# Kernel tuning notes

Measured on AMD Instinct MI355X. Metric: run time of the kernel, lower is better.

## Reference

```python
import jax, jax.numpy as jnp
import numpy as np

N, E, EL, D_IN, D_H = 100000, 1600000, 200000, 128, 128

def setup_inputs() -> dict:
    key = jax.random.key(0)
    ks = jax.random.split(key, 12)
    glorot = lambda k, fi, fo: jax.random.normal(k, (fi, fo), jnp.float32) * np.sqrt(2.0 / (fi + fo))
    return {
        "x": jax.random.normal(ks[0], (N, D_IN), jnp.float32),
        "edge_index": jax.random.randint(ks[1], (2, E), 0, N, jnp.int64),
        "edge_label_index": jax.random.randint(ks[2], (2, EL), 0, N, jnp.int64),
        "W1": glorot(ks[3], D_IN, D_H), "b1": jnp.zeros((D_H,), jnp.float32),
        "W2": glorot(ks[4], D_H, D_H), "b2": jnp.zeros((D_H,), jnp.float32),
        "Wp1": glorot(ks[5], 2 * D_H, D_H), "bp1": jnp.zeros((D_H,), jnp.float32),
        "Wp2": glorot(ks[6], D_H, 1), "bp2": jnp.zeros((1,), jnp.float32),
    }

def gcn_conv(x, W, b, src, dst, n_nodes):
    # GCNConv: h = D^{-1/2} (A + I) D^{-1/2} (x @ W) + b, deg includes self-loop
    h = x @ W                                            # [N, D]
    deg = jnp.zeros((n_nodes,), h.dtype).at[dst].add(1.0) + 1.0
    dinv = jax.lax.rsqrt(deg)                            # [N]
    coef = dinv[src] * dinv[dst]                         # [E]
    agg = jnp.zeros_like(h).at[dst].add(h[src] * coef[:, None])
    agg = agg + h * (dinv * dinv)[:, None]               # self-loop term
    return agg + b

def reference(x, edge_index, edge_label_index, W1, b1, W2, b2, Wp1, bp1, Wp2, bp2):
    src, dst = edge_index[0], edge_index[1]
    n = x.shape[0]
    h = jax.nn.relu(gcn_conv(x, W1, b1, src, dst, n))
    h = gcn_conv(h, W2, b2, src, dst, n)
    # link scoring: gather src/dst embeddings, concat, 2-layer MLP (dropout = eval identity)
    edge_emb = jnp.concatenate([h[edge_label_index[0]], h[edge_label_index[1]]], axis=1)  # [EL, 2D]
    pred = jax.nn.relu(edge_emb @ Wp1 + bp1) @ Wp2 + bp2
    return pred.squeeze(-1)
```

## Files before the change

kernel.cpp:

```cpp
#include <hip/hip_runtime.h>

#define NN 100000
#define EE 1600000
#define ELN 200000

#define NB 98
#define BKT_SHIFT 10
#define BKT_NODES 1024
#define MSB 256
#define EPB (EE / MSB)

typedef __attribute__((ext_vector_type(4))) float f32x4;
typedef __attribute__((ext_vector_type(8))) short short8;

__device__ __forceinline__ unsigned short f2bf(float f) {
    unsigned u = __builtin_bit_cast(unsigned, f);
    u += 0x7FFF + ((u >> 16) & 1);
    return (unsigned short)(u >> 16);
}
__device__ __forceinline__ float bf2f(unsigned short h) {
    return __builtin_bit_cast(float, (unsigned)h << 16);
}

__device__ __forceinline__ void convw_one(const float* __restrict__ W,
                                          unsigned short* __restrict__ WT, int K, int u) {
    int n = u & 127, kq = u >> 7;
    short8 t;
#pragma unroll
    for (int j = 0; j < 8; j++)
        t[j] = (short)f2bf(W[(size_t)(kq * 8 + j) * 128 + n]);
    *(short8*)(WT + (size_t)n * K + kq * 8) = t;
}

__global__ __launch_bounds__(256) void convw_kernel(const float* __restrict__ W1,
                                                    const float* __restrict__ W2,
                                                    const float* __restrict__ Wp1,
                                                    unsigned short* __restrict__ W1T,
                                                    unsigned short* __restrict__ W2T,
                                                    unsigned short* __restrict__ WpT) {
    int u = blockIdx.x * 256 + threadIdx.x;
    if (u < 2048) convw_one(W1, W1T, 128, u);
    else if (u < 4096) convw_one(W2, W2T, 128, u - 2048);
    else convw_one(Wp1, WpT, 256, u - 4096);
}

__global__ __launch_bounds__(256) void ms_hist_kernel(const int* __restrict__ dst,
                                                      int* __restrict__ histM) {
    __shared__ int cnt[NB];
    int tid = threadIdx.x;
    if (tid < NB) cnt[tid] = 0;
    __syncthreads();
    int base = blockIdx.x * EPB;
    for (int i = tid; i < EPB; i += 256)
        atomicAdd(&cnt[dst[base + i] >> BKT_SHIFT], 1);
    __syncthreads();
    if (tid < NB) histM[tid * MSB + blockIdx.x] = cnt[tid];
}

__global__ __launch_bounds__(256) void ms_scan_kernel(int* __restrict__ histM,
                                                      int* __restrict__ rowptr) {
    __shared__ int sm[256];
    int tid = threadIdx.x;
    const int CPT = NB * MSB / 256;
    int base = tid * CPT;
    int s = 0;
    for (int i = 0; i < CPT; i++) s += histM[base + i];
    sm[tid] = s;
    __syncthreads();
    for (int off = 1; off < 256; off <<= 1) {
        int add = (tid >= off) ? sm[tid - off] : 0;
        __syncthreads();
        sm[tid] += add;
        __syncthreads();
    }
    int run = sm[tid] - s;
    for (int i = 0; i < CPT; i++) {
        int v = histM[base + i];
        histM[base + i] = run;
        run += v;
    }
    if (tid == 0) rowptr[NN] = EE;
}

__global__ __launch_bounds__(256) void ms_scatter_kernel(const int* __restrict__ src,
                                                         const int* __restrict__ dst,
                                                         const int* __restrict__ histO,
                                                         unsigned* __restrict__ tmp) {
    __shared__ int off[NB];
    int tid = threadIdx.x;
    if (tid < NB) off[tid] = histO[tid * MSB + blockIdx.x];
    __syncthreads();
    int base = blockIdx.x * EPB;
    for (int i = tid; i < EPB; i += 256) {
        int d = dst[base + i];
        int s = src[base + i];
        int b = d >> BKT_SHIFT;
        int pos = atomicAdd(&off[b], 1);
        tmp[pos] = ((unsigned)(d & (BKT_NODES - 1)) << 17) | (unsigned)s;
    }
}

__global__ __launch_bounds__(256) void bucket_csr_kernel(const unsigned* __restrict__ tmp,
                                                         const int* __restrict__ histO,
                                                         int* __restrict__ rowptr,
                                                         float* __restrict__ dinv,
                                                         int* __restrict__ csr) {
    __shared__ int cnt[BKT_NODES];
    __shared__ int lp[BKT_NODES];
    __shared__ int sm[256];
    int b = blockIdx.x;
    int tid = threadIdx.x;
    int gbase = histO[b * MSB];
    int gend = (b == NB - 1) ? EE : histO[(b + 1) * MSB];
    for (int i = tid; i < BKT_NODES; i += 256) cnt[i] = 0;
    __syncthreads();
    for (int i = gbase + tid; i < gend; i += 256)
        atomicAdd(&cnt[tmp[i] >> 17], 1);
    __syncthreads();
    int s0 = cnt[tid * 4], s1 = cnt[tid * 4 + 1], s2 = cnt[tid * 4 + 2], s3 = cnt[tid * 4 + 3];
    int tot = s0 + s1 + s2 + s3;
    sm[tid] = tot;
    __syncthreads();
    for (int off = 1; off < 256; off <<= 1) {
        int add = (tid >= off) ? sm[tid - off] : 0;
        __syncthreads();
        sm[tid] += add;
        __syncthreads();
    }
    int excl = sm[tid] - tot;
    lp[tid * 4] = excl;
    lp[tid * 4 + 1] = excl + s0;
    lp[tid * 4 + 2] = excl + s0 + s1;
    lp[tid * 4 + 3] = excl + s0 + s1 + s2;
    int n0 = b << BKT_SHIFT;
#pragma unroll
    for (int q = 0; q < 4; q++) {
        int i = tid * 4 + q;
        int node = n0 + i;
        if (node < NN) {
            rowptr[node] = gbase + (q == 0 ? excl : lp[i]);
            int c = (q == 0) ? s0 : (q == 1 ? s1 : (q == 2 ? s2 : s3));
            dinv[node] = rsqrtf((float)c + 1.0f);
        }
    }
    cnt[tid * 4] = 0; cnt[tid * 4 + 1] = 0; cnt[tid * 4 + 2] = 0; cnt[tid * 4 + 3] = 0;
    __syncthreads();
    for (int i = gbase + tid; i < gend; i += 256) {
        unsigned p = tmp[i];
        int dl = p >> 17;
        int s = p & 0x1FFFF;
        int pos = atomicAdd(&cnt[dl], 1);
        csr[gbase + lp[dl] + pos] = s;
    }
}

template <bool A_IS_F32>
__global__ __launch_bounds__(256) void gemm_mfma_kernel(const void* __restrict__ Av,
                                                        const unsigned short* __restrict__ WT,
                                                        unsigned short* __restrict__ out,
                                                        int nrows, int nchunks) {
    __shared__ __align__(16) char Wl[128 * 128 * 2];
    int tid = threadIdx.x;
#pragma unroll
    for (int j = 0; j < 8; j++) {
        int slot = tid + j * 256;
        int n = slot >> 4, k0 = (slot & 15) * 8;
        int byte = (n * 256 + k0 * 2) ^ ((n & 7) << 4);
        *(short8*)(Wl + byte) = ((const short8*)WT)[slot];
    }
    __syncthreads();
    int wid = tid >> 6, l = tid & 63;
    int lhi = l >> 4, llo = l & 15;
    for (int chunk = blockIdx.x; chunk < nchunks; chunk += gridDim.x) {
        int r0 = chunk * 64 + wid * 16;
        int arow = r0 + llo;
        f32x4 acc[8];
#pragma unroll
        for (int c = 0; c < 8; c++) acc[c] = (f32x4)0.0f;
#pragma unroll
        for (int ks = 0; ks < 4; ks++) {
            int koff = ks * 32 + lhi * 8;
            short8 a;
            if (arow < nrows) {
                if (A_IS_F32) {
                    const float* ap = (const float*)Av + (size_t)arow * 128 + koff;
                    float4 v0 = *(const float4*)ap;
                    float4 v1 = *(const float4*)(ap + 4);
                    a[0] = (short)f2bf(v0.x); a[1] = (short)f2bf(v0.y);
                    a[2] = (short)f2bf(v0.z); a[3] = (short)f2bf(v0.w);
                    a[4] = (short)f2bf(v1.x); a[5] = (short)f2bf(v1.y);
                    a[6] = (short)f2bf(v1.z); a[7] = (short)f2bf(v1.w);
                } else {
                    a = *(const short8*)((const unsigned short*)Av + (size_t)arow * 128 + koff);
                }
            } else {
                a = (short8)(short)0;
            }
#pragma unroll
            for (int c = 0; c < 8; c++) {
                int n = c * 16 + llo;
                int byte = (n * 256 + koff * 2) ^ ((n & 7) << 4);
                short8 bfr = *(const short8*)(Wl + byte);
                acc[c] = __builtin_amdgcn_mfma_f32_16x16x32_bf16(a, bfr, acc[c], 0, 0, 0);
            }
        }
#pragma unroll
        for (int c = 0; c < 8; c++) {
            int col = c * 16 + llo;
#pragma unroll
            for (int j = 0; j < 4; j++) {
                int row = r0 + lhi * 4 + j;
                if (row < nrows) out[(size_t)row * 128 + col] = f2bf(acc[c][j]);
            }
        }
    }
}

__global__ __launch_bounds__(256) void agg_bf16_kernel(const unsigned short* __restrict__ h,
                                                       const int* __restrict__ rowptr,
                                                       const int* __restrict__ csr,
                                                       const float* __restrict__ dinv,
                                                       const float* __restrict__ bias,
                                                       unsigned short* __restrict__ out,
                                                       int relu) {
    int wid = threadIdx.x >> 6, l = threadIdx.x & 63;
    int node = blockIdx.x * 4 + wid;
    if (node >= NN) return;
    const unsigned* hp = (const unsigned*)h;
    float dn = dinv[node];
    unsigned sv = hp[(size_t)node * 64 + l];
    float a0 = bf2f((unsigned short)sv) * dn * dn;
    float a1 = bf2f((unsigned short)(sv >> 16)) * dn * dn;
    int beg = rowptr[node], end = rowptr[node + 1];
    int i = beg;
    for (; i + 8 <= end; i += 8) {
        int s[8];
        unsigned v[8];
        float c[8];
#pragma unroll
        for (int j = 0; j < 8; j++) s[j] = __builtin_nontemporal_load(csr + i + j);
#pragma unroll
        for (int j = 0; j < 8; j++) v[j] = hp[(size_t)s[j] * 64 + l];
#pragma unroll
        for (int j = 0; j < 8; j++) c[j] = dinv[s[j]] * dn;
#pragma unroll
        for (int j = 0; j < 8; j++) {
            a0 += c[j] * bf2f((unsigned short)v[j]);
            a1 += c[j] * bf2f((unsigned short)(v[j] >> 16));
        }
    }
    for (; i < end; i++) {
        int s = __builtin_nontemporal_load(csr + i);
        unsigned v = hp[(size_t)s * 64 + l];
        float c = dinv[s] * dn;
        a0 += c * bf2f((unsigned short)v);
        a1 += c * bf2f((unsigned short)(v >> 16));
    }
    a0 += bias[l * 2];
    a1 += bias[l * 2 + 1];
    if (relu) { a0 = fmaxf(a0, 0.f); a1 = fmaxf(a1, 0.f); }
    unsigned packed = (unsigned)f2bf(a0) | ((unsigned)f2bf(a1) << 16);
    __builtin_nontemporal_store(packed, (unsigned*)out + (size_t)node * 64 + l);
}

__global__ __launch_bounds__(512, 2) void link_mfma_kernel(const unsigned short* __restrict__ h,
                                                           const int* __restrict__ eli,
                                                           const unsigned short* __restrict__ WpT,
                                                           const float* __restrict__ bp1,
                                                           const float* __restrict__ Wp2,
                                                           const float* __restrict__ bp2,
                                                           float* __restrict__ out) {
    __shared__ __align__(16) char Wl[128 * 256 * 2];
    int tid = threadIdx.x;
#pragma unroll
    for (int j = 0; j < 8; j++) {
        int slot = tid + j * 512;
        int n = slot >> 5, k0 = (slot & 31) * 8;
        int byte = (n * 512 + k0 * 2) ^ ((n & 7) << 4);
        *(short8*)(Wl + byte) = ((const short8*)WpT)[slot];
    }
    __syncthreads();
    int wid = tid >> 6, l = tid & 63;
    int lhi = l >> 4, llo = l & 15;
    float b2 = bp2[0];
    const int NG = (ELN + 127) / 128;
    for (int g = blockIdx.x; g < NG; g += gridDim.x) {
        int e_base = g * 128 + wid * 16;
        if (e_base >= ELN) continue;
        int ea = e_base + llo;
        int es = eli[ea], et = eli[ELN + ea];
        f32x4 acc[8];
#pragma unroll
        for (int c = 0; c < 8; c++) acc[c] = (f32x4)0.0f;
#pragma unroll
        for (int ks = 0; ks < 8; ks++) {
            int kg = ks * 32 + lhi * 8;
            int row = (kg < 128) ? es : et;
            int koff = kg & 127;
            short8 a = *(const short8*)(h + (size_t)row * 128 + koff);
#pragma unroll
            for (int c = 0; c < 8; c++) {
                int n = c * 16 + llo;
                int byte = (n * 512 + kg * 2) ^ ((n & 7) << 4);
                short8 bfr = *(const short8*)(Wl + byte);
                acc[c] = __builtin_amdgcn_mfma_f32_16x16x32_bf16(a, bfr, acc[c], 0, 0, 0);
            }
        }
        float p0 = 0.f, p1 = 0.f, p2 = 0.f, p3 = 0.f;
#pragma unroll
        for (int c = 0; c < 8; c++) {
            int col = c * 16 + llo;
            float bb = bp1[col];
            float w2 = Wp2[col];
            p0 += fmaxf(acc[c][0] + bb, 0.f) * w2;
            p1 += fmaxf(acc[c][1] + bb, 0.f) * w2;
            p2 += fmaxf(acc[c][2] + bb, 0.f) * w2;
            p3 += fmaxf(acc[c][3] + bb, 0.f) * w2;
        }
#pragma unroll
        for (int off = 1; off < 16; off <<= 1) {
            p0 += __shfl_xor(p0, off);
            p1 += __shfl_xor(p1, off);
            p2 += __shfl_xor(p2, off);
            p3 += __shfl_xor(p3, off);
        }
        if (llo == 0) {
            int e = e_base + lhi * 4;
            out[e + 0] = p0 + b2;
            out[e + 1] = p1 + b2;
            out[e + 2] = p2 + b2;
            out[e + 3] = p3 + b2;
        }
    }
}

extern "C" void kernel_launch(void* const* d_in, const int* in_sizes, int n_in,
                              void* d_out, int out_size, void* d_ws, size_t ws_size,
                              hipStream_t stream) {
    const float* x   = (const float*)d_in[0];
    const int*   ei  = (const int*)d_in[1];
    const int*   eli = (const int*)d_in[2];
    const float* W1  = (const float*)d_in[3];
    const float* b1  = (const float*)d_in[4];
    const float* W2  = (const float*)d_in[5];
    const float* b2  = (const float*)d_in[6];
    const float* Wp1 = (const float*)d_in[7];
    const float* bp1 = (const float*)d_in[8];
    const float* Wp2 = (const float*)d_in[9];
    const float* bp2 = (const float*)d_in[10];
    float* out = (float*)d_out;

    char* w = (char*)d_ws;
    auto alloc = [&](size_t bytes) {
        char* p = w;
        w += (bytes + 255) & ~(size_t)255;
        return p;
    };
    float*          dinv   = (float*)alloc((size_t)NN * 4);
    int*            rowptr = (int*)alloc((size_t)(NN + 1) * 4);
    int*            histM  = (int*)alloc((size_t)NB * MSB * 4);
    unsigned*       tmp    = (unsigned*)alloc((size_t)EE * 4);
    int*            csr    = (int*)alloc((size_t)EE * 4);
    unsigned short* hA     = (unsigned short*)alloc((size_t)NN * 128 * 2);
    unsigned short* hB     = (unsigned short*)alloc((size_t)NN * 128 * 2);
    unsigned short* W1T    = (unsigned short*)alloc((size_t)128 * 128 * 2);
    unsigned short* W2T    = (unsigned short*)alloc((size_t)128 * 128 * 2);
    unsigned short* WpT    = (unsigned short*)alloc((size_t)128 * 256 * 2);

    const int* srcv = ei;
    const int* dstv = ei + EE;

    convw_kernel<<<32, 256, 0, stream>>>(W1, W2, Wp1, W1T, W2T, WpT);

    ms_hist_kernel<<<MSB, 256, 0, stream>>>(dstv, histM);
    ms_scan_kernel<<<1, 256, 0, stream>>>(histM, rowptr);
    ms_scatter_kernel<<<MSB, 256, 0, stream>>>(srcv, dstv, histM, tmp);
    bucket_csr_kernel<<<NB, 256, 0, stream>>>(tmp, histM, rowptr, dinv, csr);

    int nchunks = (NN + 63) / 64;
    gemm_mfma_kernel<true><<<1024, 256, 0, stream>>>(x, W1T, hA, NN, nchunks);
    agg_bf16_kernel<<<NN / 4, 256, 0, stream>>>(hA, rowptr, csr, dinv, b1, hB, 1);
    gemm_mfma_kernel<false><<<1024, 256, 0, stream>>>(hB, W2T, hA, NN, nchunks);
    agg_bf16_kernel<<<NN / 4, 256, 0, stream>>>(hA, rowptr, csr, dinv, b2, hB, 0);
    link_mfma_kernel<<<512, 512, 0, stream>>>(hB, eli, WpT, bp1, Wp2, bp2, out);
}
```

Baseline: 330.3 us.

## Pre-scale GEMM output by dinv and aggregate over feature-sliced layout

```diff
diff --git a/kernel.cpp b/kernel.cpp
--- a/kernel.cpp
+++ b/kernel.cpp
@@ -154,11 +154,12 @@
     }
 }
 
-template <bool A_IS_F32>
+template <int AMODE>
 __global__ __launch_bounds__(256) void gemm_mfma_kernel(const void* __restrict__ Av,
                                                         const unsigned short* __restrict__ WT,
+                                                        const float* __restrict__ dinv,
                                                         unsigned short* __restrict__ out,
-                                                        int nrows, int nchunks) {
+                                                        int nchunks) {
     __shared__ __align__(16) char Wl[128 * 128 * 2];
     int tid = threadIdx.x;
 #pragma unroll
@@ -181,8 +182,8 @@
         for (int ks = 0; ks < 4; ks++) {
             int koff = ks * 32 + lhi * 8;
             short8 a;
-            if (arow < nrows) {
-                if (A_IS_F32) {
+            if (arow < NN) {
+                if (AMODE == 0) {
                     const float* ap = (const float*)Av + (size_t)arow * 128 + koff;
                     float4 v0 = *(const float4*)ap;
                     float4 v1 = *(const float4*)(ap + 4);
@@ -191,7 +192,9 @@
                     a[4] = (short)f2bf(v1.x); a[5] = (short)f2bf(v1.y);
                     a[6] = (short)f2bf(v1.z); a[7] = (short)f2bf(v1.w);
                 } else {
-                    a = *(const short8*)((const unsigned short*)Av + (size_t)arow * 128 + koff);
+                    const unsigned short* gsrc = (const unsigned short*)Av;
+                    a = *(const short8*)(gsrc + (size_t)(koff >> 4) * (NN * 16) +
+                                         (size_t)arow * 16 + (koff & 15));
                 }
             } else {
                 a = (short8)(short)0;
@@ -204,63 +207,75 @@
                 acc[c] = __builtin_amdgcn_mfma_f32_16x16x32_bf16(a, bfr, acc[c], 0, 0, 0);
             }
         }
+        float dv[4];
+#pragma unroll
+        for (int j = 0; j < 4; j++) {
+            int row = r0 + lhi * 4 + j;
+            dv[j] = (row < NN) ? dinv[row] : 0.f;
+        }
 #pragma unroll
         for (int c = 0; c < 8; c++) {
-            int col = c * 16 + llo;
 #pragma unroll
             for (int j = 0; j < 4; j++) {
                 int row = r0 + lhi * 4 + j;
-                if (row < nrows) out[(size_t)row * 128 + col] = f2bf(acc[c][j]);
+                if (row < NN)
+                    out[(size_t)c * (NN * 16) + (size_t)row * 16 + llo] = f2bf(acc[c][j] * dv[j]);
             }
         }
     }
 }
 
-__global__ __launch_bounds__(256) void agg_bf16_kernel(const unsigned short* __restrict__ h,
-                                                       const int* __restrict__ rowptr,
-                                                       const int* __restrict__ csr,
-                                                       const float* __restrict__ dinv,
-                                                       const float* __restrict__ bias,
-                                                       unsigned short* __restrict__ out,
-                                                       int relu) {
-    int wid = threadIdx.x >> 6, l = threadIdx.x & 63;
-    int node = blockIdx.x * 4 + wid;
-    if (node >= NN) return;
-    const unsigned* hp = (const unsigned*)h;
-    float dn = dinv[node];
-    unsigned sv = hp[(size_t)node * 64 + l];
-    float a0 = bf2f((unsigned short)sv) * dn * dn;
-    float a1 = bf2f((unsigned short)(sv >> 16)) * dn * dn;
-    int beg = rowptr[node], end = rowptr[node + 1];
-    int i = beg;
-    for (; i + 8 <= end; i += 8) {
-        int s[8];
-        unsigned v[8];
-        float c[8];
-#pragma unroll
-        for (int j = 0; j < 8; j++) s[j] = __builtin_nontemporal_load(csr + i + j);
-#pragma unroll
-        for (int j = 0; j < 8; j++) v[j] = hp[(size_t)s[j] * 64 + l];
-#pragma unroll
-        for (int j = 0; j < 8; j++) c[j] = dinv[s[j]] * dn;
-#pragma unroll
-        for (int j = 0; j < 8; j++) {
-            a0 += c[j] * bf2f((unsigned short)v[j]);
-            a1 += c[j] * bf2f((unsigned short)(v[j] >> 16));
-        }
-    }
-    for (; i < end; i++) {
-        int s = __builtin_nontemporal_load(csr + i);
-        unsigned v = hp[(size_t)s * 64 + l];
-        float c = dinv[s] * dn;
-        a0 += c * bf2f((unsigned short)v);
-        a1 += c * bf2f((unsigned short)(v >> 16));
-    }
-    a0 += bias[l * 2];
-    a1 += bias[l * 2 + 1];
-    if (relu) { a0 = fmaxf(a0, 0.f); a1 = fmaxf(a1, 0.f); }
-    unsigned packed = (unsigned)f2bf(a0) | ((unsigned)f2bf(a1) << 16);
-    __builtin_nontemporal_store(packed, (unsigned*)out + (size_t)node * 64 + l);
+template <int OUT_ROW>
+__global__ __launch_bounds__(512) void agg_fs_kernel(const unsigned short* __restrict__ g,
+                                                     const int* __restrict__ rowptr,
+                                                     const int* __restrict__ csr,
+                                                     const float* __restrict__ dinv,
+                                                     const float* __restrict__ bias,
+                                                     unsigned short* __restrict__ out) {
+    int s = blockIdx.x & 7;
+    int nb = blockIdx.x >> 3;
+    int w = threadIdx.x >> 6;
+    int l = threadIdx.x & 63;
+    int j = l >> 3, d = l & 7;
+    const unsigned* gp = (const unsigned*)g + (size_t)s * (NN * 8);
+    float bb0 = bias[s * 16 + d * 2];
+    float bb1 = bias[s * 16 + d * 2 + 1];
+#pragma unroll
+    for (int t = 0; t < 4; t++) {
+        int node = nb * 32 + w * 4 + t;
+        float a0 = 0.f, a1 = 0.f;
+        int beg = rowptr[node], end = rowptr[node + 1];
+        for (int i = beg + j; i < end; i += 16) {
+            int s0 = csr[i];
+            int i1 = i + 8;
+            int s1 = (i1 < end) ? csr[i1] : -1;
+            unsigned v0 = gp[(size_t)s0 * 8 + d];
+            a0 += bf2f((unsigned short)v0);
+            a1 += bf2f((unsigned short)(v0 >> 16));
+            if (s1 >= 0) {
+                unsigned v1 = gp[(size_t)s1 * 8 + d];
+                a0 += bf2f((unsigned short)v1);
+                a1 += bf2f((unsigned short)(v1 >> 16));
+            }
+        }
+        a0 += __shfl_xor(a0, 8);  a1 += __shfl_xor(a1, 8);
+        a0 += __shfl_xor(a0, 16); a1 += __shfl_xor(a1, 16);
+        a0 += __shfl_xor(a0, 32); a1 += __shfl_xor(a1, 32);
+        unsigned sv = gp[(size_t)node * 8 + d];
+        a0 += bf2f((unsigned short)sv);
+        a1 += bf2f((unsigned short)(sv >> 16));
+        float dn = dinv[node];
+        a0 = fmaf(dn, a0, bb0);
+        a1 = fmaf(dn, a1, bb1);
+        if (!OUT_ROW) { a0 = fmaxf(a0, 0.f); a1 = fmaxf(a1, 0.f); }
+        if (j == 0) {
+            unsigned packed = (unsigned)f2bf(a0) | ((unsigned)f2bf(a1) << 16);
+            if (OUT_ROW)
+                ((unsigned*)out)[(size_t)node * 64 + s * 8 + d] = packed;
+            else
+                ((unsigned*)out)[(size_t)s * (NN * 8) + (size_t)node * 8 + d] = packed;
+        }
+    }
 }
 
 __global__ __launch_bounds__(512, 2) void link_mfma_kernel(const unsigned short* __restrict__ h,
@@ -361,8 +376,8 @@
     int*            histM  = (int*)alloc((size_t)NB * MSB * 4);
     unsigned*       tmp    = (unsigned*)alloc((size_t)EE * 4);
     int*            csr    = (int*)alloc((size_t)EE * 4);
-    unsigned short* hA     = (unsigned short*)alloc((size_t)NN * 128 * 2);
-    unsigned short* hB     = (unsigned short*)alloc((size_t)NN * 128 * 2);
+    unsigned short* gbuf   = (unsigned short*)alloc((size_t)NN * 128 * 2);
+    unsigned short* hbuf   = (unsigned short*)alloc((size_t)NN * 128 * 2);
     unsigned short* W1T    = (unsigned short*)alloc((size_t)128 * 128 * 2);
     unsigned short* W2T    = (unsigned short*)alloc((size_t)128 * 128 * 2);
     unsigned short* WpT    = (unsigned short*)alloc((size_t)128 * 256 * 2);
@@ -378,9 +393,9 @@
     bucket_csr_kernel<<<NB, 256, 0, stream>>>(tmp, histM, rowptr, dinv, csr);
 
     int nchunks = (NN + 63) / 64;
-    gemm_mfma_kernel<true><<<1024, 256, 0, stream>>>(x, W1T, hA, NN, nchunks);
-    agg_bf16_kernel<<<NN / 4, 256, 0, stream>>>(hA, rowptr, csr, dinv, b1, hB, 1);
-    gemm_mfma_kernel<false><<<1024, 256, 0, stream>>>(hB, W2T, hA, NN, nchunks);
-    agg_bf16_kernel<<<NN / 4, 256, 0, stream>>>(hA, rowptr, csr, dinv, b2, hB, 0);
-    link_mfma_kernel<<<512, 512, 0, stream>>>(hB, eli, WpT, bp1, Wp2, bp2, out);
-}
+    gemm_mfma_kernel<0><<<1024, 256, 0, stream>>>(x, W1T, dinv, gbuf, nchunks);
+    agg_fs_kernel<0><<<25000, 512, 0, stream>>>(gbuf, rowptr, csr, dinv, b1, hbuf);
+    gemm_mfma_kernel<1><<<1024, 256, 0, stream>>>(hbuf, W2T, dinv, gbuf, nchunks);
+    agg_fs_kernel<1><<<25000, 512, 0, stream>>>(gbuf, rowptr, csr, dinv, b2, hbuf);
+    link_mfma_kernel<<<512, 512, 0, stream>>>(hbuf, eli, WpT, bp1, Wp2, bp2, out);
+}
```

After: 542.7 us. 64.3% more time.
